# Kernel tuning notes

Hardware: AMD Instinct MI355X
Metric: run time of the kernel (lower is better)

The kernel has to match this reference:

```python
import jax, jax.numpy as jnp
import numpy as np

N = 100000
E = 3200000
IN_DIM = 128
HID = 64
BN_EPS = 1e-5


def _gcn_conv(x, W, b, src, dst, dinv):
    h = x @ W                                      # [N, out]
    coeff = (dinv[src] * dinv[dst])[:, None]       # [E, 1]
    msg = h[src] * coeff                           # gather over edges
    agg = jax.ops.segment_sum(msg, dst, num_segments=N)
    agg = agg + h * (dinv * dinv)[:, None]         # self-loop term
    return agg + b


def setup_inputs() -> dict:
    key = jax.random.key(0)
    ks = jax.random.split(key, 12)
    x = jax.random.normal(ks[0], (N, IN_DIM), dtype=jnp.float32)
    edge_index = jax.random.randint(ks[1], (2, E), 0, N, dtype=jnp.int64)
    s1 = 1.0 / np.sqrt(IN_DIM)
    s2 = 1.0 / np.sqrt(HID)
    W1 = jax.random.uniform(ks[2], (IN_DIM, HID), jnp.float32, -s1, s1)
    b1 = jnp.zeros((HID,), jnp.float32)
    W2 = jax.random.uniform(ks[3], (HID, HID), jnp.float32, -s2, s2)
    b2 = jnp.zeros((HID,), jnp.float32)
    W3 = jax.random.uniform(ks[4], (HID, 1), jnp.float32, -s2, s2)
    b3 = jnp.zeros((1,), jnp.float32)
    g1 = jnp.ones((HID,), jnp.float32)
    beta1 = jnp.zeros((HID,), jnp.float32)
    m1 = 0.1 * jax.random.normal(ks[5], (HID,), jnp.float32)
    v1 = jax.random.uniform(ks[6], (HID,), jnp.float32) + 0.5
    g2 = jnp.ones((HID,), jnp.float32)
    beta2 = jnp.zeros((HID,), jnp.float32)
    m2 = 0.1 * jax.random.normal(ks[7], (HID,), jnp.float32)
    v2 = jax.random.uniform(ks[8], (HID,), jnp.float32) + 0.5
    return {"x": x, "edge_index": edge_index,
            "W1": W1, "b1": b1, "W2": W2, "b2": b2, "W3": W3, "b3": b3,
            "g1": g1, "beta1": beta1, "m1": m1, "v1": v1,
            "g2": g2, "beta2": beta2, "m2": m2, "v2": v2}


def reference(x, edge_index, W1, b1, W2, b2, W3, b3,
              g1, beta1, m1, v1, g2, beta2, m2, v2):
    src, dst = edge_index[0], edge_index[1]
    # degree with self-loops (computed on destination index, PyG convention)
    deg = jax.ops.segment_sum(jnp.ones((E,), jnp.float32), dst, num_segments=N) + 1.0
    dinv = jax.lax.rsqrt(deg)

    def bn(h, g, beta, m, v):
        return (h - m) * jax.lax.rsqrt(v + BN_EPS) * g + beta

    h = _gcn_conv(x, W1, b1, src, dst, dinv)
    h = jax.nn.relu(bn(h, g1, beta1, m1, v1))  # dropout is a no-op in eval
    h = _gcn_conv(h, W2, b2, src, dst, dinv)
    h = jax.nn.relu(bn(h, g2, beta2, m2, v2))
    h = _gcn_conv(h, W3, b3, src, dst, dinv)
    return jax.nn.sigmoid(h)  # [N, 1]
```

## Files before the change

kernel.cpp:

```cpp
#include <hip/hip_runtime.h>
#include <math.h>

#define N_NODES 100000
#define E_EDGES 3200000
#define IN_DIM_ 128
#define HID_ 64
#define BN_EPS_ 1e-5f

#define PB 200
#define CHUNK 16000
#define NBUCK 391

typedef __attribute__((ext_vector_type(8))) short short8;
typedef __attribute__((ext_vector_type(4))) float f32x4;

__device__ inline ushort f2bf(float f) {
    union { float f; unsigned u; } c; c.f = f;
    unsigned r = c.u + 0x7fff + ((c.u >> 16) & 1);
    return (ushort)(r >> 16);
}

__global__ __launch_bounds__(256) void passA1_hist(const int* __restrict__ ei,
                                                   int* __restrict__ histPB) {
    __shared__ int hist[NBUCK];
    int t = threadIdx.x, b = blockIdx.x;
    for (int k = t; k < NBUCK; k += 256) hist[k] = 0;
    __syncthreads();
    int e0 = b * CHUNK, e1 = e0 + CHUNK;
    for (int e = e0 + t; e < e1; e += 256) {
        int d = ei[E_EDGES + e];
        atomicAdd(&hist[d >> 8], 1);
    }
    __syncthreads();
    for (int k = t; k < NBUCK; k += 256) histPB[k * PB + b] = hist[k];
}

__global__ __launch_bounds__(256) void scan_rows(int* __restrict__ histPB,
                                                 int* __restrict__ bucket_tot) {
    __shared__ int wsum[4];
    int k = blockIdx.x, t = threadIdx.x, lane = t & 63, wv = t >> 6;
    int v = (t < PB) ? histPB[k * PB + t] : 0;
    int s = v;
#pragma unroll
    for (int off = 1; off < 64; off <<= 1) {
        int u = __shfl_up(s, off, 64);
        if (lane >= off) s += u;
    }
    if (lane == 63) wsum[wv] = s;
    __syncthreads();
    int wbase = 0;
    for (int w = 0; w < wv; w++) wbase += wsum[w];
    if (t < PB) histPB[k * PB + t] = wbase + s - v;
    if (t == 255) bucket_tot[k] = wbase + s;
}

__global__ __launch_bounds__(512) void scan_totals(const int* __restrict__ bucket_tot,
                                                   int* __restrict__ bucket_base,
                                                   int* __restrict__ row_ptr) {
    __shared__ int wsum[8];
    int t = threadIdx.x, lane = t & 63, wv = t >> 6;
    int v = (t < NBUCK) ? bucket_tot[t] : 0;
    int s = v;
#pragma unroll
    for (int off = 1; off < 64; off <<= 1) {
        int u = __shfl_up(s, off, 64);
        if (lane >= off) s += u;
    }
    if (lane == 63) wsum[wv] = s;
    __syncthreads();
    int wbase = 0;
    for (int w = 0; w < wv; w++) wbase += wsum[w];
    if (t < NBUCK) bucket_base[t] = wbase + s - v;
    if (t == 0) {
        bucket_base[NBUCK] = E_EDGES;
        row_ptr[N_NODES] = E_EDGES;
    }
}

__global__ __launch_bounds__(256) void passA2_scatter(const int* __restrict__ ei,
                                                      const int* __restrict__ histPB,
                                                      const int* __restrict__ bucket_base,
                                                      int* __restrict__ ebuf) {
    __shared__ int cur[NBUCK];
    int t = threadIdx.x, b = blockIdx.x;
    for (int k = t; k < NBUCK; k += 256) cur[k] = bucket_base[k] + histPB[k * PB + b];
    __syncthreads();
    int e0 = b * CHUNK, e1 = e0 + CHUNK;
    for (int e = e0 + t; e < e1; e += 256) {
        int s = ei[e];
        int d = ei[E_EDGES + e];
        int bk = d >> 8;
        int pos = atomicAdd(&cur[bk], 1);
        ebuf[pos] = s | ((d & 255) << 17);
    }
}

__global__ __launch_bounds__(256) void passB_place(const int* __restrict__ ebuf,
                                                   const int* __restrict__ bucket_base,
                                                   int* __restrict__ row_ptr,
                                                   int* __restrict__ csr_src,
                                                   float* __restrict__ dinv) {
    __shared__ int hist[256];
    __shared__ int wsum[4];
    int b = blockIdx.x, t = threadIdx.x, lane = t & 63, wv = t >> 6;
    int base = bucket_base[b], end = bucket_base[b + 1];
    hist[t] = 0;
    __syncthreads();
    for (int k = base + t; k < end; k += 256)
        atomicAdd(&hist[ebuf[k] >> 17], 1);
    __syncthreads();
    int v = hist[t];
    int s = v;
#pragma unroll
    for (int off = 1; off < 64; off <<= 1) {
        int u = __shfl_up(s, off, 64);
        if (lane >= off) s += u;
    }
    if (lane == 63) wsum[wv] = s;
    __syncthreads();
    int wbase = 0;
    for (int w = 0; w < wv; w++) wbase += wsum[w];
    int excl = wbase + s - v;
    int node = b * 256 + t;
    if (node < N_NODES) {
        row_ptr[node] = base + excl;
        dinv[node] = rsqrtf((float)v + 1.0f);
    }
    __syncthreads();
    hist[t] = excl;
    __syncthreads();
    for (int k = base + t; k < end; k += 256) {
        int pv = ebuf[k];
        int pos = atomicAdd(&hist[pv >> 17], 1);
        csr_src[base + pos] = pv & 0x1FFFF;
    }
}

template<int K>
__global__ __launch_bounds__(256) void gemm_bf16(const float* __restrict__ X,
                                                 const float* __restrict__ W,
                                                 const float* __restrict__ dinv,
                                                 ushort* __restrict__ hs) {
    constexpr int KP = K + 8;
    constexpr int K4 = K / 4;
    __shared__ ushort A_lds[64][KP];
    __shared__ ushort Wt_lds[64][KP];
    int t = threadIdx.x;
    long row0 = (long)blockIdx.x * 64;

    for (int i = t; i < K * 64; i += 256) {
        int k = i >> 6, n = i & 63;
        Wt_lds[n][k] = f2bf(W[i]);
    }
    for (int i = t; i < 64 * K4; i += 256) {
        int r = i / K4, c = i % K4;
        float4 val = make_float4(0.f, 0.f, 0.f, 0.f);
        long row = row0 + r;
        if (row < N_NODES) val = ((const float4*)X)[row * K4 + c];
        int cb = c * 4;
        A_lds[r][cb + 0] = f2bf(val.x);
        A_lds[r][cb + 1] = f2bf(val.y);
        A_lds[r][cb + 2] = f2bf(val.z);
        A_lds[r][cb + 3] = f2bf(val.w);
    }
    __syncthreads();

    int w = t >> 6, l = t & 63;
    int m = l & 15, quad = l >> 4;
    f32x4 acc[4];
#pragma unroll
    for (int c = 0; c < 4; c++) acc[c] = (f32x4){0.f, 0.f, 0.f, 0.f};

#pragma unroll
    for (int ch = 0; ch < K / 32; ch++) {
        short8 a = *(const short8*)&A_lds[16 * w + m][32 * ch + 8 * quad];
#pragma unroll
        for (int c = 0; c < 4; c++) {
            short8 b = *(const short8*)&Wt_lds[16 * c + m][32 * ch + 8 * quad];
            acc[c] = __builtin_amdgcn_mfma_f32_16x16x32_bf16(a, b, acc[c], 0, 0, 0);
        }
    }

#pragma unroll
    for (int r = 0; r < 4; r++) {
        long node = row0 + 16 * w + quad * 4 + r;
        if (node < N_NODES) {
            float dv = dinv[node];
#pragma unroll
            for (int c = 0; c < 4; c++)
                hs[node * 64 + 16 * c + m] = f2bf(acc[c][r] * dv);
        }
    }
}

__global__ __launch_bounds__(256) void gather_feat(const int* __restrict__ row_ptr,
                                                   const int* __restrict__ csr_src,
                                                   const ushort* __restrict__ hs,
                                                   const float* __restrict__ dinv,
                                                   const float* __restrict__ b,
                                                   const float* __restrict__ g,
                                                   const float* __restrict__ beta,
                                                   const float* __restrict__ m,
                                                   const float* __restrict__ v,
                                                   float* __restrict__ y, int n) {
    int i = (blockIdx.x * 256 + threadIdx.x) >> 6;
    if (i >= n) return;
    int l = threadIdx.x & 63;
    int half = l >> 5, u = l & 31;
    const unsigned* H = (const unsigned*)hs;
    int beg = row_ptr[i], end = row_ptr[i + 1];
    float a0 = 0.f, a1 = 0.f;
    int k = beg + half;
    for (; k + 2 < end; k += 4) {
        int s0 = csr_src[k], s1 = csr_src[k + 2];
        unsigned p0 = H[s0 * 32 + u], p1 = H[s1 * 32 + u];
        union { unsigned u; float f; } c0, c1, c2, c3;
        c0.u = p0 << 16; c1.u = p0 & 0xffff0000u;
        c2.u = p1 << 16; c3.u = p1 & 0xffff0000u;
        a0 += c0.f + c2.f;
        a1 += c1.f + c3.f;
    }
    for (; k < end; k += 2) {
        unsigned p = H[csr_src[k] * 32 + u];
        union { unsigned u; float f; } cl, ch;
        cl.u = p << 16; ch.u = p & 0xffff0000u;
        a0 += cl.f; a1 += ch.f;
    }
    a0 += __shfl_xor(a0, 32, 64);
    a1 += __shfl_xor(a1, 32, 64);
    unsigned ps = H[(long)i * 32 + u];
    union { unsigned u; float f; } sl, sh;
    sl.u = ps << 16; sh.u = ps & 0xffff0000u;
    a0 += sl.f; a1 += sh.f;

    float2 bb = ((const float2*)b)[u];
    float2 gg = ((const float2*)g)[u];
    float2 be = ((const float2*)beta)[u];
    float2 mm = ((const float2*)m)[u];
    float2 vv = ((const float2*)v)[u];
    float di = dinv[i];
    float s0 = gg.x * rsqrtf(vv.x + BN_EPS_);
    float s1 = gg.y * rsqrtf(vv.y + BN_EPS_);
    float o0 = fmaxf((di * a0 + bb.x - mm.x) * s0 + be.x, 0.f);
    float o1 = fmaxf((di * a1 + bb.y - mm.y) * s1 + be.y, 0.f);
    if (half == 0) ((float2*)y)[(long)i * 32 + u] = make_float2(o0, o1);
}

__global__ __launch_bounds__(256) void gemv3(const float* __restrict__ y2,
                                             const float* __restrict__ W3,
                                             const float* __restrict__ dinv,
                                             float* __restrict__ hs3) {
    int t = blockIdx.x * 256 + threadIdx.x;
    int i = t >> 6, j = t & 63;
    float p = y2[t] * W3[j];
#pragma unroll
    for (int off = 32; off > 0; off >>= 1)
        p += __shfl_down(p, off, 64);
    if (j == 0) hs3[i] = p * dinv[i];
}

__global__ __launch_bounds__(256) void gather3(const int* __restrict__ row_ptr,
                                               const int* __restrict__ csr_src,
                                               const float* __restrict__ hs3,
                                               const float* __restrict__ dinv,
                                               const float* __restrict__ b3,
                                               float* __restrict__ out, int n) {
    int i = blockIdx.x * 256 + threadIdx.x;
    if (i >= n) return;
    int beg = row_ptr[i], end = row_ptr[i + 1];
    float s0 = hs3[i], s1 = 0.f, s2 = 0.f, s3 = 0.f;
    int k = beg;
    for (; k + 4 <= end; k += 4) {
        s0 += hs3[csr_src[k]];
        s1 += hs3[csr_src[k + 1]];
        s2 += hs3[csr_src[k + 2]];
        s3 += hs3[csr_src[k + 3]];
    }
    for (; k < end; k++) s0 += hs3[csr_src[k]];
    float z = dinv[i] * ((s0 + s1) + (s2 + s3)) + b3[0];
    out[i] = 1.f / (1.f + expf(-z));
}

extern "C" void kernel_launch(void* const* d_in, const int* in_sizes, int n_in,
                              void* d_out, int out_size, void* d_ws, size_t ws_size,
                              hipStream_t stream) {
    const int N = N_NODES;
    const int E = E_EDGES;

    const float* x   = (const float*)d_in[0];
    const int*   ei  = (const int*)d_in[1];
    const float* W1  = (const float*)d_in[2];
    const float* b1  = (const float*)d_in[3];
    const float* W2  = (const float*)d_in[4];
    const float* b2  = (const float*)d_in[5];
    const float* W3  = (const float*)d_in[6];
    const float* b3  = (const float*)d_in[7];
    const float* g1  = (const float*)d_in[8];
    const float* bt1 = (const float*)d_in[9];
    const float* m1  = (const float*)d_in[10];
    const float* v1  = (const float*)d_in[11];
    const float* g2  = (const float*)d_in[12];
    const float* bt2 = (const float*)d_in[13];
    const float* m2  = (const float*)d_in[14];
    const float* v2  = (const float*)d_in[15];
    float* out = (float*)d_out;

    int*   wsi         = (int*)d_ws;
    float* dinv        = (float*)wsi;
    float* hs3         = (float*)(wsi + (long)N);
    int*   row_ptr     = wsi + 2L * N;
    int*   histPB      = wsi + 3L * N + 16;
    int*   bucket_tot  = histPB + NBUCK * PB;
    int*   bucket_base = bucket_tot + 400;
    int*   csr_src     = bucket_base + 400;
    ushort* hsb        = (ushort*)(csr_src + (long)E);
    float* B           = (float*)(csr_src + (long)E + 32L * N);
    int*   ebuf        = (int*)hsb;

    passA1_hist<<<PB, 256, 0, stream>>>(ei, histPB);
    scan_rows<<<NBUCK, 256, 0, stream>>>(histPB, bucket_tot);
    scan_totals<<<1, 512, 0, stream>>>(bucket_tot, bucket_base, row_ptr);
    passA2_scatter<<<PB, 256, 0, stream>>>(ei, histPB, bucket_base, ebuf);
    passB_place<<<NBUCK, 256, 0, stream>>>(ebuf, bucket_base, row_ptr, csr_src, dinv);

    gemm_bf16<IN_DIM_><<<(N + 63) / 64, 256, 0, stream>>>(x, W1, dinv, hsb);
    gather_feat<<<N / 4, 256, 0, stream>>>(row_ptr, csr_src, hsb, dinv,
                                           b1, g1, bt1, m1, v1, B, N);
    gemm_bf16<HID_><<<(N + 63) / 64, 256, 0, stream>>>(B, W2, dinv, hsb);
    gather_feat<<<N / 4, 256, 0, stream>>>(row_ptr, csr_src, hsb, dinv,
                                           b2, g2, bt2, m2, v2, B, N);
    gemv3<<<(N * HID_) / 256, 256, 0, stream>>>(B, W3, dinv, hs3);
    gather3<<<(N + 255) / 256, 256, 0, stream>>>(row_ptr, csr_src, hs3, dinv, b3, out, N);
}
```

Measured before the change: 473.9 us.

## Fuse layer-3 GEMV into gather, store intermediate features as bf16, deepen unrolls

Folds the W3 matrix-vector product into the second gather kernel, so its output never goes to memory and one kernel launch is dropped. The first gather now writes bf16-packed activations, which the second GEMM loads directly without an fp32 read and conversion. Also vectorizes the W load with float4, unrolls the edge gather loops to four and eight independent loads, and adds more accumulators in gather3 for memory-level parallelism. Rounding the intermediate activations to bf16 is the only extra precision cost, since the GEMM already converted its input to bf16.

```diff
diff --git a/kernel.cpp b/kernel.cpp
--- a/kernel.cpp
+++ b/kernel.cpp
@@ -19,6 +19,8 @@
     unsigned r = c.u + 0x7fff + ((c.u >> 16) & 1);
     return (ushort)(r >> 16);
 }
+__device__ inline float bf_lo(unsigned p) { union { unsigned u; float f; } c; c.u = p << 16; return c.f; }
+__device__ inline float bf_hi(unsigned p) { union { unsigned u; float f; } c; c.u = p & 0xffff0000u; return c.f; }
 
 __global__ __launch_bounds__(256) void passA1_hist(const int* __restrict__ ei,
                                                    int* __restrict__ histPB) {
@@ -136,32 +138,49 @@
     }
 }
 
-template<int K>
-__global__ __launch_bounds__(256) void gemm_bf16(const float* __restrict__ X,
+template<int K, bool BF16IN>
+__global__ __launch_bounds__(256) void gemm_bf16(const void* __restrict__ Xv,
                                                  const float* __restrict__ W,
                                                  const float* __restrict__ dinv,
                                                  ushort* __restrict__ hs) {
     constexpr int KP = K + 8;
-    constexpr int K4 = K / 4;
     __shared__ ushort A_lds[64][KP];
     __shared__ ushort Wt_lds[64][KP];
     int t = threadIdx.x;
     long row0 = (long)blockIdx.x * 64;
 
-    for (int i = t; i < K * 64; i += 256) {
-        int k = i >> 6, n = i & 63;
-        Wt_lds[n][k] = f2bf(W[i]);
-    }
-    for (int i = t; i < 64 * K4; i += 256) {
-        int r = i / K4, c = i % K4;
-        float4 val = make_float4(0.f, 0.f, 0.f, 0.f);
-        long row = row0 + r;
-        if (row < N_NODES) val = ((const float4*)X)[row * K4 + c];
-        int cb = c * 4;
-        A_lds[r][cb + 0] = f2bf(val.x);
-        A_lds[r][cb + 1] = f2bf(val.y);
-        A_lds[r][cb + 2] = f2bf(val.z);
-        A_lds[r][cb + 3] = f2bf(val.w);
+    for (int i = t; i < K * 16; i += 256) {
+        float4 w4 = ((const float4*)W)[i];
+        int k = i >> 4, n = (i & 15) * 4;
+        Wt_lds[n + 0][k] = f2bf(w4.x);
+        Wt_lds[n + 1][k] = f2bf(w4.y);
+        Wt_lds[n + 2][k] = f2bf(w4.z);
+        Wt_lds[n + 3][k] = f2bf(w4.w);
+    }
+    if (BF16IN) {
+        constexpr int K2 = K / 2;
+        const unsigned* X = (const unsigned*)Xv;
+        for (int i = t; i < 64 * K2; i += 256) {
+            int r = i / K2, c = i % K2;
+            unsigned val = 0;
+            long row = row0 + r;
+            if (row < N_NODES) val = X[row * K2 + c];
+            *(unsigned*)&A_lds[r][c * 2] = val;
+        }
+    } else {
+        constexpr int K4 = K / 4;
+        const float* X = (const float*)Xv;
+        for (int i = t; i < 64 * K4; i += 256) {
+            int r = i / K4, c = i % K4;
+            float4 val = make_float4(0.f, 0.f, 0.f, 0.f);
+            long row = row0 + r;
+            if (row < N_NODES) val = ((const float4*)X)[row * K4 + c];
+            int cb = c * 4;
+            A_lds[r][cb + 0] = f2bf(val.x);
+            A_lds[r][cb + 1] = f2bf(val.y);
+            A_lds[r][cb + 2] = f2bf(val.z);
+            A_lds[r][cb + 3] = f2bf(val.w);
+        }
     }
     __syncthreads();
 
@@ -193,6 +212,7 @@
     }
 }
 
+template<bool LAST>
 __global__ __launch_bounds__(256) void gather_feat(const int* __restrict__ row_ptr,
                                                    const int* __restrict__ csr_src,
                                                    const ushort* __restrict__ hs,
@@ -202,7 +222,9 @@
                                                    const float* __restrict__ beta,
                                                    const float* __restrict__ m,
                                                    const float* __restrict__ v,
-                                                   float* __restrict__ y, int n) {
+                                                   unsigned* __restrict__ y,
+                                                   const float* __restrict__ W3,
+                                                   float* __restrict__ hs3, int n) {
     int i = (blockIdx.x * 256 + threadIdx.x) >> 6;
     if (i >= n) return;
     int l = threadIdx.x & 63;
@@ -211,27 +233,23 @@
     int beg = row_ptr[i], end = row_ptr[i + 1];
     float a0 = 0.f, a1 = 0.f;
     int k = beg + half;
-    for (; k + 2 < end; k += 4) {
-        int s0 = csr_src[k], s1 = csr_src[k + 2];
+    for (; k + 6 < end; k += 8) {
+        int s0 = csr_src[k], s1 = csr_src[k + 2], s2 = csr_src[k + 4], s3 = csr_src[k + 6];
         unsigned p0 = H[s0 * 32 + u], p1 = H[s1 * 32 + u];
-        union { unsigned u; float f; } c0, c1, c2, c3;
-        c0.u = p0 << 16; c1.u = p0 & 0xffff0000u;
-        c2.u = p1 << 16; c3.u = p1 & 0xffff0000u;
-        a0 += c0.f + c2.f;
-        a1 += c1.f + c3.f;
+        unsigned p2 = H[s2 * 32 + u], p3 = H[s3 * 32 + u];
+        a0 += (bf_lo(p0) + bf_lo(p1)) + (bf_lo(p2) + bf_lo(p3));
+        a1 += (bf_hi(p0) + bf_hi(p1)) + (bf_hi(p2) + bf_hi(p3));
     }
     for (; k < end; k += 2) {
         unsigned p = H[csr_src[k] * 32 + u];
-        union { unsigned u; float f; } cl, ch;
-        cl.u = p << 16; ch.u = p & 0xffff0000u;
-        a0 += cl.f; a1 += ch.f;
+        a0 += bf_lo(p);
+        a1 += bf_hi(p);
     }
     a0 += __shfl_xor(a0, 32, 64);
     a1 += __shfl_xor(a1, 32, 64);
     unsigned ps = H[(long)i * 32 + u];
-    union { unsigned u; float f; } sl, sh;
-    sl.u = ps << 16; sh.u = ps & 0xffff0000u;
-    a0 += sl.f; a1 += sh.f;
+    a0 += bf_lo(ps);
+    a1 += bf_hi(ps);
 
     float2 bb = ((const float2*)b)[u];
     float2 gg = ((const float2*)g)[u];
@@ -243,20 +261,18 @@
     float s1 = gg.y * rsqrtf(vv.y + BN_EPS_);
     float o0 = fmaxf((di * a0 + bb.x - mm.x) * s0 + be.x, 0.f);
     float o1 = fmaxf((di * a1 + bb.y - mm.y) * s1 + be.y, 0.f);
-    if (half == 0) ((float2*)y)[(long)i * 32 + u] = make_float2(o0, o1);
-}
-
-__global__ __launch_bounds__(256) void gemv3(const float* __restrict__ y2,
-                                             const float* __restrict__ W3,
-                                             const float* __restrict__ dinv,
-                                             float* __restrict__ hs3) {
-    int t = blockIdx.x * 256 + threadIdx.x;
-    int i = t >> 6, j = t & 63;
-    float p = y2[t] * W3[j];
-#pragma unroll
-    for (int off = 32; off > 0; off >>= 1)
-        p += __shfl_down(p, off, 64);
-    if (j == 0) hs3[i] = p * dinv[i];
+
+    if (LAST) {
+        float2 w3 = ((const float2*)W3)[u];
+        float p = o0 * w3.x + o1 * w3.y;
+#pragma unroll
+        for (int off = 16; off > 0; off >>= 1)
+            p += __shfl_down(p, off, 32);
+        if (l == 0) hs3[i] = p * di;
+    } else {
+        if (half == 0)
+            y[(long)i * 32 + u] = (unsigned)f2bf(o0) | ((unsigned)f2bf(o1) << 16);
+    }
 }
 
 __global__ __launch_bounds__(256) void gather3(const int* __restrict__ row_ptr,
@@ -269,15 +285,20 @@
     if (i >= n) return;
     int beg = row_ptr[i], end = row_ptr[i + 1];
     float s0 = hs3[i], s1 = 0.f, s2 = 0.f, s3 = 0.f;
+    float s4 = 0.f, s5 = 0.f, s6 = 0.f, s7 = 0.f;
     int k = beg;
-    for (; k + 4 <= end; k += 4) {
+    for (; k + 8 <= end; k += 8) {
         s0 += hs3[csr_src[k]];
         s1 += hs3[csr_src[k + 1]];
         s2 += hs3[csr_src[k + 2]];
         s3 += hs3[csr_src[k + 3]];
+        s4 += hs3[csr_src[k + 4]];
+        s5 += hs3[csr_src[k + 5]];
+        s6 += hs3[csr_src[k + 6]];
+        s7 += hs3[csr_src[k + 7]];
     }
     for (; k < end; k++) s0 += hs3[csr_src[k]];
-    float z = dinv[i] * ((s0 + s1) + (s2 + s3)) + b3[0];
+    float z = dinv[i] * (((s0 + s1) + (s2 + s3)) + ((s4 + s5) + (s6 + s7))) + b3[0];
     out[i] = 1.f / (1.f + expf(-z));
 }
 
@@ -305,17 +326,17 @@
     const float* v2  = (const float*)d_in[15];
     float* out = (float*)d_out;
 
-    int*   wsi         = (int*)d_ws;
-    float* dinv        = (float*)wsi;
-    float* hs3         = (float*)(wsi + (long)N);
-    int*   row_ptr     = wsi + 2L * N;
-    int*   histPB      = wsi + 3L * N + 16;
-    int*   bucket_tot  = histPB + NBUCK * PB;
-    int*   bucket_base = bucket_tot + 400;
-    int*   csr_src     = bucket_base + 400;
-    ushort* hsb        = (ushort*)(csr_src + (long)E);
-    float* B           = (float*)(csr_src + (long)E + 32L * N);
-    int*   ebuf        = (int*)hsb;
+    int*    wsi         = (int*)d_ws;
+    float*  dinv        = (float*)wsi;
+    float*  hs3         = (float*)(wsi + (long)N);
+    int*    row_ptr     = wsi + 2L * N;
+    int*    histPB      = wsi + 3L * N + 16;
+    int*    bucket_tot  = histPB + NBUCK * PB;
+    int*    bucket_base = bucket_tot + 400;
+    int*    csr_src     = bucket_base + 400;
+    ushort* hsb         = (ushort*)(csr_src + (long)E);
+    unsigned* yb        = (unsigned*)(csr_src + (long)E + 32L * N);
+    int*    ebuf        = (int*)hsb;
 
     passA1_hist<<<PB, 256, 0, stream>>>(ei, histPB);
     scan_rows<<<NBUCK, 256, 0, stream>>>(histPB, bucket_tot);
@@ -323,12 +344,11 @@
     passA2_scatter<<<PB, 256, 0, stream>>>(ei, histPB, bucket_base, ebuf);
     passB_place<<<NBUCK, 256, 0, stream>>>(ebuf, bucket_base, row_ptr, csr_src, dinv);
 
-    gemm_bf16<IN_DIM_><<<(N + 63) / 64, 256, 0, stream>>>(x, W1, dinv, hsb);
-    gather_feat<<<N / 4, 256, 0, stream>>>(row_ptr, csr_src, hsb, dinv,
-                                           b1, g1, bt1, m1, v1, B, N);
-    gemm_bf16<HID_><<<(N + 63) / 64, 256, 0, stream>>>(B, W2, dinv, hsb);
-    gather_feat<<<N / 4, 256, 0, stream>>>(row_ptr, csr_src, hsb, dinv,
-                                           b2, g2, bt2, m2, v2, B, N);
-    gemv3<<<(N * HID_) / 256, 256, 0, stream>>>(B, W3, dinv, hs3);
+    gemm_bf16<IN_DIM_, false><<<(N + 63) / 64, 256, 0, stream>>>(x, W1, dinv, hsb);
+    gather_feat<false><<<N / 4, 256, 0, stream>>>(row_ptr, csr_src, hsb, dinv,
+                                                  b1, g1, bt1, m1, v1, yb, W3, hs3, N);
+    gemm_bf16<HID_, true><<<(N + 63) / 64, 256, 0, stream>>>(yb, W2, dinv, hsb);
+    gather_feat<true><<<N / 4, 256, 0, stream>>>(row_ptr, csr_src, hsb, dinv,
+                                                 b2, g2, bt2, m2, v2, yb, W3, hs3, N);
     gather3<<<(N + 255) / 256, 256, 0, stream>>>(row_ptr, csr_src, hs3, dinv, b3, out, N);
 }
```

New measurement: 435.1 us. -8.2%, faster.
